# Performance work log

Measured on AMD Instinct MI355X. Metric: run time of the kernel, lower is better.

## Reference

```python
import jax, jax.numpy as jnp
import numpy as np

N = 200000      # active voxels
K = 27          # kernel volume (3x3x3)
M = 50000       # rulebook pairs per kernel offset
CIN = 64
COUT = 64


def setup_inputs() -> dict:
    key = jax.random.key(0)
    k1, k2, k3, k4 = jax.random.split(key, 4)
    feats = jax.random.normal(k1, (N, CIN), dtype=jnp.float32)
    std = 1.0 / np.sqrt(CIN * K)
    kernel = jax.random.uniform(k2, (K, CIN, COUT), dtype=jnp.float32,
                                minval=-std, maxval=std)
    in_map = jax.random.randint(k3, (K, M), 0, N, dtype=jnp.int32)
    out_map = jax.random.randint(k4, (K, M), 0, N, dtype=jnp.int32)
    return {"feats": feats, "kernel": kernel, "in_map": in_map, "out_map": out_map}


def reference(feats, kernel, in_map, out_map):
    # gather: [K, M, Cin]
    gathered = feats[in_map]
    # per-offset GEMM: [K, M, Cout]
    partial = jnp.einsum('kmi,kio->kmo', gathered, kernel)
    # scatter-add into output features [N, Cout]
    out = jnp.zeros((feats.shape[0], kernel.shape[-1]), dtype=feats.dtype)
    out = out.at[out_map].add(partial)
    return out
```

## Files before the change

kernel.cpp:

```cpp
#include <hip/hip_runtime.h>

#define CIN  64
#define COUT 64

typedef __attribute__((ext_vector_type(8))) short bf16x8;
typedef __attribute__((ext_vector_type(4))) float f32x4;

__global__ __launch_bounds__(256)
void zero_out_kernel(float4* __restrict__ out, int n4) {
    int i = blockIdx.x * 256 + threadIdx.x;
    if (i < n4) out[i] = make_float4(0.f, 0.f, 0.f, 0.f);
}

__device__ inline unsigned short f2bf(float f) {
    unsigned u = __float_as_uint(f);
    return (unsigned short)((u + 0x7FFFu + ((u >> 16) & 1u)) >> 16);
}

__global__ __launch_bounds__(256)
void spconv_mfma(const float* __restrict__ feats,
                 const float* __restrict__ weight,
                 const int*   __restrict__ in_map,
                 const int*   __restrict__ out_map,
                 float*       __restrict__ out,
                 int M) {
    const int k     = blockIdx.y;
    const int tid   = threadIdx.x;
    const int lane  = tid & 63;
    const int m     = lane & 15;
    const int quad  = lane >> 4;
    const int wave  = blockIdx.x * 4 + (tid >> 6);
    const int nwaves = gridDim.x * 4;

    const float* __restrict__ wk = weight + (size_t)k * (CIN * COUT);
    bf16x8 bfrag[4][2];
#pragma unroll
    for (int t = 0; t < 4; ++t) {
#pragma unroll
        for (int h = 0; h < 2; ++h) {
            const int n = 16 * t + m;
            const int c0 = 32 * h + 8 * quad;
#pragma unroll
            for (int j = 0; j < 8; ++j)
                bfrag[t][h][j] = (short)f2bf(wk[(c0 + j) * COUT + n]);
        }
    }

    const int base   = k * M;
    const int ntiles = M >> 4;

    for (int tile = wave; tile < ntiles; tile += nwaves) {
        const int p0 = tile << 4;

        const int in_row  = in_map[base + p0 + m];
        const int out_row = out_map[base + p0 + m];

        const float* __restrict__ fr = feats + (size_t)in_row * CIN + 8 * quad;
        const f32x4 f0 = *(const f32x4*)(fr + 0);
        const f32x4 f1 = *(const f32x4*)(fr + 4);
        const f32x4 f2 = *(const f32x4*)(fr + 32);
        const f32x4 f3 = *(const f32x4*)(fr + 36);

        bf16x8 a0, a1;
#pragma unroll
        for (int j = 0; j < 4; ++j) {
            a0[j]     = (short)f2bf(f0[j]);
            a0[j + 4] = (short)f2bf(f1[j]);
            a1[j]     = (short)f2bf(f2[j]);
            a1[j + 4] = (short)f2bf(f3[j]);
        }

        int orow[4];
#pragma unroll
        for (int r = 0; r < 4; ++r)
            orow[r] = __shfl(out_row, 4 * quad + r);

        f32x4 acc[4];
#pragma unroll
        for (int t = 0; t < 4; ++t) {
            acc[t] = {0.f, 0.f, 0.f, 0.f};
            acc[t] = __builtin_amdgcn_mfma_f32_16x16x32_bf16(a0, bfrag[t][0], acc[t], 0, 0, 0);
            acc[t] = __builtin_amdgcn_mfma_f32_16x16x32_bf16(a1, bfrag[t][1], acc[t], 0, 0, 0);
        }

#pragma unroll
        for (int t = 0; t < 4; ++t)
#pragma unroll
            for (int r = 0; r < 4; ++r)
                atomicAdd(out + (size_t)orow[r] * COUT + 16 * t + m, acc[t][r]);
    }
}

extern "C" void kernel_launch(void* const* d_in, const int* in_sizes, int n_in,
                              void* d_out, int out_size, void* d_ws, size_t ws_size,
                              hipStream_t stream) {
    const float* feats   = (const float*)d_in[0];
    const float* weight  = (const float*)d_in[1];
    const int*   in_map  = (const int*)d_in[2];
    const int*   out_map = (const int*)d_in[3];
    float*       out     = (float*)d_out;

    const int K = in_sizes[1] / (CIN * COUT);
    const int M = in_sizes[2] / K;

    {
        int n4 = out_size / 4;
        zero_out_kernel<<<(n4 + 255) / 256, 256, 0, stream>>>((float4*)out, n4);
    }

    dim3 grid(64, K);
    spconv_mfma<<<grid, 256, 0, stream>>>(feats, weight, in_map, out_map, out, M);
}
```

Measured before the change: 377.6 us.

## Pair lanes via shuffles to issue packed two-float atomic adds

Adjacent lanes swap accumulator values with xor-shuffles so each lane holds two consecutive output columns for one row. Each lane then issues a packed v2f32 global atomic add, halving the number of atomic operations per tile. The change also replaces the custom zeroing kernel with hipMemsetAsync and raises the grid from 64 to 80 blocks per kernel offset. In exchange it adds shuffle and select overhead, and on toolchains without the builtin it falls back to two scalar atomics.

```diff
diff --git a/kernel.cpp b/kernel.cpp
--- a/kernel.cpp
+++ b/kernel.cpp
@@ -5,16 +5,22 @@
 
 typedef __attribute__((ext_vector_type(8))) short bf16x8;
 typedef __attribute__((ext_vector_type(4))) float f32x4;
-
-__global__ __launch_bounds__(256)
-void zero_out_kernel(float4* __restrict__ out, int n4) {
-    int i = blockIdx.x * 256 + threadIdx.x;
-    if (i < n4) out[i] = make_float4(0.f, 0.f, 0.f, 0.f);
-}
+typedef __attribute__((ext_vector_type(2))) float f32x2;
 
 __device__ inline unsigned short f2bf(float f) {
     unsigned u = __float_as_uint(f);
     return (unsigned short)((u + 0x7FFFu + ((u >> 16) & 1u)) >> 16);
+}
+
+__device__ inline void atomic_pk_add(float* addr, f32x2 v) {
+#if __has_builtin(__builtin_amdgcn_global_atomic_fadd_v2f32)
+    typedef __attribute__((address_space(1))) f32x2 gf32x2;
+    __builtin_amdgcn_global_atomic_fadd_v2f32(
+        (gf32x2*)(unsigned long long)(void*)addr, v);
+#else
+    atomicAdd(addr + 0, v.x);
+    atomicAdd(addr + 1, v.y);
+#endif
 }
 
 __global__ __launch_bounds__(256)
@@ -83,11 +89,26 @@
             acc[t] = __builtin_amdgcn_mfma_f32_16x16x32_bf16(a1, bfrag[t][1], acc[t], 0, 0, 0);
         }
 
+        const bool odd = (m & 1);
 #pragma unroll
-        for (int t = 0; t < 4; ++t)
-#pragma unroll
-            for (int r = 0; r < 4; ++r)
-                atomicAdd(out + (size_t)orow[r] * COUT + 16 * t + m, acc[t][r]);
+        for (int t = 0; t < 4; ++t) {
+            const float pv0 = __shfl_xor(acc[t][0], 1);
+            const float pv1 = __shfl_xor(acc[t][1], 1);
+            const float pv2 = __shfl_xor(acc[t][2], 1);
+            const float pv3 = __shfl_xor(acc[t][3], 1);
+            const int colb = 16 * t + (m & ~1);
+
+            const int ra = odd ? orow[2] : orow[0];
+            const int rb = odd ? orow[3] : orow[1];
+            f32x2 va, vb;
+            va.x = odd ? pv2       : acc[t][0];
+            va.y = odd ? acc[t][2] : pv0;
+            vb.x = odd ? pv3       : acc[t][1];
+            vb.y = odd ? acc[t][3] : pv1;
+
+            atomic_pk_add(out + (size_t)ra * COUT + colb, va);
+            atomic_pk_add(out + (size_t)rb * COUT + colb, vb);
+        }
     }
 }
 
@@ -103,11 +124,8 @@
     const int K = in_sizes[1] / (CIN * COUT);
     const int M = in_sizes[2] / K;
 
-    {
-        int n4 = out_size / 4;
-        zero_out_kernel<<<(n4 + 255) / 256, 256, 0, stream>>>((float4*)out, n4);
-    }
+    hipMemsetAsync(out, 0, (size_t)out_size * sizeof(float), stream);
 
-    dim3 grid(64, K);
+    dim3 grid(80, K);
     spconv_mfma<<<grid, 256, 0, stream>>>(feats, weight, in_map, out_map, out, M);
 }
```

Result: slower. 651.4 us (+72.5%).

## Replace atomic scatter-add with inverse-index gather using fp16 partials

Applied to the files above, without the earlier changes.

Builds an inverse rulebook (a per-output-row count plus a capped pair list) with a cheap atomic pass. Phase 1 computes the per-pair GEMM with MFMA and stores the results as fp16 partials in the workspace. Phase 2 has one wave per output row sum its partials and write the row once, which removes the zeroing pass and the per-element float atomics. In exchange the code writes and reads a large partial buffer, loses precision by storing partials in fp16, and silently drops any contributions past CAP=48 per output row. It falls back to the atomic path when the workspace is too small.

```diff
diff --git a/kernel.cpp b/kernel.cpp
--- a/kernel.cpp
+++ b/kernel.cpp
@@ -1,16 +1,12 @@
 #include <hip/hip_runtime.h>
+#include <hip/hip_fp16.h>
 
 #define CIN  64
 #define COUT 64
+#define CAP  48
 
 typedef __attribute__((ext_vector_type(8))) short bf16x8;
 typedef __attribute__((ext_vector_type(4))) float f32x4;
-
-__global__ __launch_bounds__(256)
-void zero_out_kernel(float4* __restrict__ out, int n4) {
-    int i = blockIdx.x * 256 + threadIdx.x;
-    if (i < n4) out[i] = make_float4(0.f, 0.f, 0.f, 0.f);
-}
 
 __device__ inline unsigned short f2bf(float f) {
     unsigned u = __float_as_uint(f);
@@ -18,42 +14,48 @@
 }
 
 __global__ __launch_bounds__(256)
-void spconv_mfma(const float* __restrict__ feats,
-                 const float* __restrict__ weight,
-                 const int*   __restrict__ in_map,
-                 const int*   __restrict__ out_map,
-                 float*       __restrict__ out,
-                 int M) {
-    const int k     = blockIdx.y;
-    const int tid   = threadIdx.x;
-    const int lane  = tid & 63;
-    const int m     = lane & 15;
-    const int quad  = lane >> 4;
-    const int wave  = blockIdx.x * 4 + (tid >> 6);
+void build_inverse(const int* __restrict__ out_map, int total,
+                   int* __restrict__ cnt, int* __restrict__ pairlist) {
+    int g = blockIdx.x * 256 + threadIdx.x;
+    if (g >= total) return;
+    int r = out_map[g];
+    int pos = atomicAdd(&cnt[r], 1);
+    if (pos < CAP) pairlist[r * CAP + pos] = g;
+}
+
+__global__ __launch_bounds__(256)
+void spconv_phase1(const float* __restrict__ feats,
+                   const float* __restrict__ weight,
+                   const int*   __restrict__ in_map,
+                   __half*      __restrict__ partial,
+                   int M) {
+    const int k      = blockIdx.y;
+    const int tid    = threadIdx.x;
+    const int lane   = tid & 63;
+    const int m      = lane & 15;
+    const int quad   = lane >> 4;
+    const int wave   = blockIdx.x * 4 + (tid >> 6);
     const int nwaves = gridDim.x * 4;
 
     const float* __restrict__ wk = weight + (size_t)k * (CIN * COUT);
     bf16x8 bfrag[4][2];
 #pragma unroll
-    for (int t = 0; t < 4; ++t) {
+    for (int t = 0; t < 4; ++t)
 #pragma unroll
         for (int h = 0; h < 2; ++h) {
-            const int n = 16 * t + m;
+            const int n  = 16 * t + m;
             const int c0 = 32 * h + 8 * quad;
 #pragma unroll
             for (int j = 0; j < 8; ++j)
                 bfrag[t][h][j] = (short)f2bf(wk[(c0 + j) * COUT + n]);
         }
-    }
 
     const int base   = k * M;
     const int ntiles = M >> 4;
 
     for (int tile = wave; tile < ntiles; tile += nwaves) {
         const int p0 = tile << 4;
-
-        const int in_row  = in_map[base + p0 + m];
-        const int out_row = out_map[base + p0 + m];
+        const int in_row = in_map[base + p0 + m];
 
         const float* __restrict__ fr = feats + (size_t)in_row * CIN + 8 * quad;
         const f32x4 f0 = *(const f32x4*)(fr + 0);
@@ -70,11 +72,6 @@
             a1[j + 4] = (short)f2bf(f3[j]);
         }
 
-        int orow[4];
-#pragma unroll
-        for (int r = 0; r < 4; ++r)
-            orow[r] = __shfl(out_row, 4 * quad + r);
-
         f32x4 acc[4];
 #pragma unroll
         for (int t = 0; t < 4; ++t) {
@@ -83,12 +80,118 @@
             acc[t] = __builtin_amdgcn_mfma_f32_16x16x32_bf16(a1, bfrag[t][1], acc[t], 0, 0, 0);
         }
 
+        const size_t tbase = ((size_t)(k * ntiles + tile) << 10) + 256 * quad + m;
+#pragma unroll
+        for (int t = 0; t < 4; ++t)
+#pragma unroll
+            for (int r = 0; r < 4; ++r)
+                partial[tbase + 64 * r + 16 * t] = __float2half(acc[t][r]);
+    }
+}
+
+__global__ __launch_bounds__(256)
+void spconv_phase2(const __half* __restrict__ partial,
+                   const int*    __restrict__ cnt,
+                   const int*    __restrict__ pairlist,
+                   float*        __restrict__ out,
+                   int nrows) {
+    const int lane   = threadIdx.x & 63;
+    const int wave   = blockIdx.x * 4 + (threadIdx.x >> 6);
+    const int nwaves = gridDim.x * 4;
+
+    for (int r = wave; r < nrows; r += nwaves) {
+        int c = cnt[r];
+        if (c > CAP) c = CAP;
+        const int* __restrict__ pl = pairlist + r * CAP;
+
+        float acc = 0.f;
+        for (int j = 0; j < c; ++j) {
+            const int e   = pl[j];
+            const int r15 = e & 15;
+            const size_t elem = ((size_t)(e >> 4) << 10)
+                              + 256 * (r15 >> 2) + 64 * (r15 & 3) + lane;
+            acc += __half2float(partial[elem]);
+        }
+        out[(size_t)r * COUT + lane] = acc;
+    }
+}
+
+__global__ __launch_bounds__(256)
+void spconv_atomic(const float* __restrict__ feats,
+                   const float* __restrict__ weight,
+                   const int*   __restrict__ in_map,
+                   const int*   __restrict__ out_map,
+                   float*       __restrict__ out,
+                   int M) {
+    const int k      = blockIdx.y;
+    const int tid    = threadIdx.x;
+    const int lane   = tid & 63;
+    const int m      = lane & 15;
+    const int quad   = lane >> 4;
+    const int wave   = blockIdx.x * 4 + (tid >> 6);
+    const int nwaves = gridDim.x * 4;
+
+    const float* __restrict__ wk = weight + (size_t)k * (CIN * COUT);
+    bf16x8 bfrag[4][2];
+#pragma unroll
+    for (int t = 0; t < 4; ++t)
+#pragma unroll
+        for (int h = 0; h < 2; ++h) {
+            const int n  = 16 * t + m;
+            const int c0 = 32 * h + 8 * quad;
+#pragma unroll
+            for (int j = 0; j < 8; ++j)
+                bfrag[t][h][j] = (short)f2bf(wk[(c0 + j) * COUT + n]);
+        }
+
+    const int base   = k * M;
+    const int ntiles = M >> 4;
+
+    for (int tile = wave; tile < ntiles; tile += nwaves) {
+        const int p0 = tile << 4;
+        const int in_row  = in_map[base + p0 + m];
+        const int out_row = out_map[base + p0 + m];
+
+        const float* __restrict__ fr = feats + (size_t)in_row * CIN + 8 * quad;
+        const f32x4 f0 = *(const f32x4*)(fr + 0);
+        const f32x4 f1 = *(const f32x4*)(fr + 4);
+        const f32x4 f2 = *(const f32x4*)(fr + 32);
+        const f32x4 f3 = *(const f32x4*)(fr + 36);
+
+        bf16x8 a0, a1;
+#pragma unroll
+        for (int j = 0; j < 4; ++j) {
+            a0[j]     = (short)f2bf(f0[j]);
+            a0[j + 4] = (short)f2bf(f1[j]);
+            a1[j]     = (short)f2bf(f2[j]);
+            a1[j + 4] = (short)f2bf(f3[j]);
+        }
+
+        int orow[4];
+#pragma unroll
+        for (int r = 0; r < 4; ++r)
+            orow[r] = __shfl(out_row, 4 * quad + r);
+
+        f32x4 acc[4];
+#pragma unroll
+        for (int t = 0; t < 4; ++t) {
+            acc[t] = {0.f, 0.f, 0.f, 0.f};
+            acc[t] = __builtin_amdgcn_mfma_f32_16x16x32_bf16(a0, bfrag[t][0], acc[t], 0, 0, 0);
+            acc[t] = __builtin_amdgcn_mfma_f32_16x16x32_bf16(a1, bfrag[t][1], acc[t], 0, 0, 0);
+        }
+
 #pragma unroll
         for (int t = 0; t < 4; ++t)
 #pragma unroll
             for (int r = 0; r < 4; ++r)
                 atomicAdd(out + (size_t)orow[r] * COUT + 16 * t + m, acc[t][r]);
     }
+}
+
+__global__ __launch_bounds__(256)
+void zero_out_kernel(float4* __restrict__ out, int n4) {
+    int i = blockIdx.x * 256 + threadIdx.x;
+    if (i < n4) out[i] = make_float4(0.f, 0.f, 0.f, 0.f);
 }
 
 extern "C" void kernel_launch(void* const* d_in, const int* in_sizes, int n_in,
@@ -100,14 +203,35 @@
     const int*   out_map = (const int*)d_in[3];
     float*       out     = (float*)d_out;
 
-    const int K = in_sizes[1] / (CIN * COUT);
-    const int M = in_sizes[2] / K;
-
-    {
+    const int K     = in_sizes[1] / (CIN * COUT);
+    const int M     = in_sizes[2] / K;
+    const int N     = out_size / COUT;
+    const int total = K * M;
+
+    const size_t cnt_b  = ((size_t)N * 4 + 255) & ~(size_t)255;
+    const size_t pl_b   = ((size_t)N * CAP * 4 + 255) & ~(size_t)255;
+    const size_t part_b = (size_t)total * COUT * sizeof(__half);
+    const size_t need   = cnt_b + pl_b + part_b;
+
+    if ((M & 15) == 0 && ws_size >= need) {
+        int*    cnt      = (int*)d_ws;
+        int*    pairlist = (int*)((char*)d_ws + cnt_b);
+        __half* partial  = (__half*)((char*)d_ws + cnt_b + pl_b);
+
+        hipMemsetAsync(cnt, 0, (size_t)N * 4, stream);
+
+        build_inverse<<<(total + 255) / 256, 256, 0, stream>>>(
+            out_map, total, cnt, pairlist);
+
+        dim3 g1(80, K);
+        spconv_phase1<<<g1, 256, 0, stream>>>(feats, weight, in_map, partial, M);
+
+        spconv_phase2<<<2048, 256, 0, stream>>>(partial, cnt, pairlist, out, N);
+    } else {
         int n4 = out_size / 4;
         zero_out_kernel<<<(n4 + 255) / 256, 256, 0, stream>>>((float4*)out, n4);
-    }
-
-    dim3 grid(64, K);
-    spconv_mfma<<<grid, 256, 0, stream>>>(feats, weight, in_map, out_map, out, M);
-}
+        dim3 grid(80, K);
+        spconv_atomic<<<grid, 256, 0, stream>>>(
+            feats, weight, in_map, out_map, out, M);
+    }
+}
```

Result: slower. 510.2 us (+35.1%).

## Accumulate scatter-add in packed fp16 atomics with pre-converted bf16 features

Applied to the files above, without the earlier changes.

Adds a path that first converts all features to bf16 in workspace, then runs the MFMA gather-GEMM and scatters results with packed v2f16 global atomics into an fp16 accumulator, which is converted back to fp32 at the end. Lanes exchange values via shuffles so each atomic carries two adjacent output columns, halving the number of atomics and the bytes moved in gathers and scatters. The grid also grows from 64 to 80 blocks per offset. It adds extra conversion passes and a memset, and fp16 accumulation risks precision loss and overflow relative to the fp32 reference.

```diff
diff --git a/kernel.cpp b/kernel.cpp
--- a/kernel.cpp
+++ b/kernel.cpp
@@ -1,16 +1,18 @@
 #include <hip/hip_runtime.h>
-
-#define CIN  64
-#define COUT 64
-
-typedef __attribute__((ext_vector_type(8))) short bf16x8;
-typedef __attribute__((ext_vector_type(4))) float f32x4;
-
-__global__ __launch_bounds__(256)
-void zero_out_kernel(float4* __restrict__ out, int n4) {
-    int i = blockIdx.x * 256 + threadIdx.x;
-    if (i < n4) out[i] = make_float4(0.f, 0.f, 0.f, 0.f);
-}
+#include <hip/hip_fp16.h>
+
+#define CIN   64
+#define COUT  64
+
+typedef __attribute__((ext_vector_type(8))) short    bf16x8;
+typedef __attribute__((ext_vector_type(4))) float    f32x4;
+typedef __attribute__((ext_vector_type(2))) _Float16 f16x2;
+
+#if __has_builtin(__builtin_amdgcn_global_atomic_fadd_v2f16)
+#define HAVE_PK16 1
+#else
+#define HAVE_PK16 0
+#endif
 
 __device__ inline unsigned short f2bf(float f) {
     unsigned u = __float_as_uint(f);
@@ -18,44 +20,147 @@
 }
 
 __global__ __launch_bounds__(256)
-void spconv_mfma(const float* __restrict__ feats,
-                 const float* __restrict__ weight,
-                 const int*   __restrict__ in_map,
-                 const int*   __restrict__ out_map,
-                 float*       __restrict__ out,
-                 int M) {
-    const int k     = blockIdx.y;
-    const int tid   = threadIdx.x;
-    const int lane  = tid & 63;
-    const int m     = lane & 15;
-    const int quad  = lane >> 4;
-    const int wave  = blockIdx.x * 4 + (tid >> 6);
+void cvt_feats(const float4* __restrict__ in, unsigned short* __restrict__ outb,
+               int n8) {
+    int i = blockIdx.x * 256 + threadIdx.x;
+    if (i >= n8) return;
+    float4 f0 = in[2 * i], f1 = in[2 * i + 1];
+    bf16x8 o;
+    o[0] = (short)f2bf(f0.x); o[1] = (short)f2bf(f0.y);
+    o[2] = (short)f2bf(f0.z); o[3] = (short)f2bf(f0.w);
+    o[4] = (short)f2bf(f1.x); o[5] = (short)f2bf(f1.y);
+    o[6] = (short)f2bf(f1.z); o[7] = (short)f2bf(f1.w);
+    *(bf16x8*)(outb + 8 * (size_t)i) = o;
+}
+
+__global__ __launch_bounds__(256)
+void cvt_out(const __half2* __restrict__ hacc, float2* __restrict__ out, int n2) {
+    int i = blockIdx.x * 256 + threadIdx.x;
+    if (i >= n2) return;
+    const __half2 h = hacc[i];
+    out[i] = make_float2(__half2float(__low2half(h)), __half2float(__high2half(h)));
+}
+
+#if HAVE_PK16
+__global__ __launch_bounds__(256)
+void spconv_pk(const unsigned short* __restrict__ featsb,
+               const float*          __restrict__ weight,
+               const int*            __restrict__ in_map,
+               const int*            __restrict__ out_map,
+               __half*               __restrict__ hacc,
+               int M) {
+    const int k      = blockIdx.y;
+    const int tid    = threadIdx.x;
+    const int lane   = tid & 63;
+    const int m      = lane & 15;
+    const int quad   = lane >> 4;
+    const int wave   = blockIdx.x * 4 + (tid >> 6);
     const int nwaves = gridDim.x * 4;
+    const bool odd   = (m & 1);
 
     const float* __restrict__ wk = weight + (size_t)k * (CIN * COUT);
     bf16x8 bfrag[4][2];
 #pragma unroll
-    for (int t = 0; t < 4; ++t) {
+    for (int t = 0; t < 4; ++t)
 #pragma unroll
         for (int h = 0; h < 2; ++h) {
-            const int n = 16 * t + m;
+            const int n  = 16 * t + m;
             const int c0 = 32 * h + 8 * quad;
 #pragma unroll
             for (int j = 0; j < 8; ++j)
                 bfrag[t][h][j] = (short)f2bf(wk[(c0 + j) * COUT + n]);
         }
-    }
 
     const int base   = k * M;
     const int ntiles = M >> 4;
 
+    typedef __attribute__((address_space(1))) f16x2 gf16x2;
+    f16x2* const hacc2 = (f16x2*)hacc;
+
+    for (int tile = wave; tile < ntiles; tile += nwaves) {
+        const int p0      = tile << 4;
+        const int in_row  = in_map[base + p0 + m];
+        const int out_row = out_map[base + p0 + m];
+
+        const unsigned short* fb = featsb + ((size_t)in_row << 6) + 8 * quad;
+        const bf16x8 a0 = *(const bf16x8*)fb;
+        const bf16x8 a1 = *(const bf16x8*)(fb + 32);
+
+        int orow[4];
+#pragma unroll
+        for (int r = 0; r < 4; ++r)
+            orow[r] = __shfl(out_row, 4 * quad + r);
+
+        f32x4 acc[4];
+#pragma unroll
+        for (int t = 0; t < 4; ++t) {
+            acc[t] = {0.f, 0.f, 0.f, 0.f};
+            acc[t] = __builtin_amdgcn_mfma_f32_16x16x32_bf16(a0, bfrag[t][0], acc[t], 0, 0, 0);
+            acc[t] = __builtin_amdgcn_mfma_f32_16x16x32_bf16(a1, bfrag[t][1], acc[t], 0, 0, 0);
+        }
+
+        const int coldw = m >> 1;
+        const int ra = odd ? orow[2] : orow[0];
+        const int rb = odd ? orow[3] : orow[1];
+#pragma unroll
+        for (int t = 0; t < 4; ++t) {
+            const float send0 = odd ? acc[t][0] : acc[t][2];
+            const float send1 = odd ? acc[t][1] : acc[t][3];
+            const float recv0 = __shfl_xor(send0, 1);
+            const float recv1 = __shfl_xor(send1, 1);
+
+            f16x2 va, vb;
+            va[0] = (_Float16)(odd ? recv0 : acc[t][0]);
+            va[1] = (_Float16)(odd ? acc[t][2] : recv0);
+            vb[0] = (_Float16)(odd ? recv1 : acc[t][1]);
+            vb[1] = (_Float16)(odd ? acc[t][3] : recv1);
+
+            __builtin_amdgcn_global_atomic_fadd_v2f16(
+                (gf16x2*)(unsigned long long)(void*)&hacc2[(size_t)ra * 32 + coldw + 8 * t], va);
+            __builtin_amdgcn_global_atomic_fadd_v2f16(
+                (gf16x2*)(unsigned long long)(void*)&hacc2[(size_t)rb * 32 + coldw + 8 * t], vb);
+        }
+    }
+}
+#endif
+
+__global__ __launch_bounds__(256)
+void spconv_atomic(const float* __restrict__ feats,
+                   const float* __restrict__ weight,
+                   const int*   __restrict__ in_map,
+                   const int*   __restrict__ out_map,
+                   float*       __restrict__ out,
+                   int M) {
+    const int k      = blockIdx.y;
+    const int tid    = threadIdx.x;
+    const int lane   = tid & 63;
+    const int m      = lane & 15;
+    const int quad   = lane >> 4;
+    const int wave   = blockIdx.x * 4 + (tid >> 6);
+    const int nwaves = gridDim.x * 4;
+
+    const float* __restrict__ wk = weight + (size_t)k * (CIN * COUT);
+    bf16x8 bfrag[4][2];
+#pragma unroll
+    for (int t = 0; t < 4; ++t)
+#pragma unroll
+        for (int h = 0; h < 2; ++h) {
+            const int n  = 16 * t + m;
+            const int c0 = 32 * h + 8 * quad;
+#pragma unroll
+            for (int j = 0; j < 8; ++j)
+                bfrag[t][h][j] = (short)f2bf(wk[(c0 + j) * COUT + n]);
+        }
+
+    const int base   = k * M;
+    const int ntiles = M >> 4;
+
     for (int tile = wave; tile < ntiles; tile += nwaves) {
         const int p0 = tile << 4;
-
         const int in_row  = in_map[base + p0 + m];
         const int out_row = out_map[base + p0 + m];
 
-        const float* __restrict__ fr = feats + (size_t)in_row * CIN + 8 * quad;
+        const float* __restrict__ fr = feats + ((size_t)in_row << 6) + 8 * quad;
         const f32x4 f0 = *(const f32x4*)(fr + 0);
         const f32x4 f1 = *(const f32x4*)(fr + 4);
         const f32x4 f2 = *(const f32x4*)(fr + 32);
@@ -89,6 +194,12 @@
             for (int r = 0; r < 4; ++r)
                 atomicAdd(out + (size_t)orow[r] * COUT + 16 * t + m, acc[t][r]);
     }
+}
+
+__global__ __launch_bounds__(256)
+void zero_out_kernel(float4* __restrict__ out, int n4) {
+    int i = blockIdx.x * 256 + threadIdx.x;
+    if (i < n4) out[i] = make_float4(0.f, 0.f, 0.f, 0.f);
 }
 
 extern "C" void kernel_launch(void* const* d_in, const int* in_sizes, int n_in,
@@ -102,12 +213,35 @@
 
     const int K = in_sizes[1] / (CIN * COUT);
     const int M = in_sizes[2] / K;
-
-    {
-        int n4 = out_size / 4;
-        zero_out_kernel<<<(n4 + 255) / 256, 256, 0, stream>>>((float4*)out, n4);
+    const int N = out_size / COUT;
+
+    const size_t fb_b   = ((size_t)N * CIN * 2 + 255) & ~(size_t)255;
+    const size_t hacc_b = (size_t)N * COUT * 2;
+    const size_t need   = fb_b + hacc_b;
+
+#if HAVE_PK16
+    if ((M & 15) == 0 && ws_size >= need) {
+        unsigned short* featsb = (unsigned short*)d_ws;
+        __half*         hacc   = (__half*)((char*)d_ws + fb_b);
+
+        hipMemsetAsync(hacc, 0, hacc_b, stream);
+
+        const int n8 = N * CIN / 8;
+        cvt_feats<<<(n8 + 255) / 256, 256, 0, stream>>>(
+            (const float4*)feats, featsb, n8);
+
+        dim3 grid(80, K);
+        spconv_pk<<<grid, 256, 0, stream>>>(featsb, weight, in_map, out_map,
+                                            hacc, M);
+
+        const int n2 = N * COUT / 2;
+        cvt_out<<<(n2 + 255) / 256, 256, 0, stream>>>(
+            (const __half2*)hacc, (float2*)out, n2);
+        return;
     }
-
-    dim3 grid(64, K);
-    spconv_mfma<<<grid, 256, 0, stream>>>(feats, weight, in_map, out_map, out, M);
-}
+#endif
+    int n4 = out_size / 4;
+    zero_out_kernel<<<(n4 + 255) / 256, 256, 0, stream>>>((float4*)out, n4);
+    dim3 grid(80, K);
+    spconv_atomic<<<grid, 256, 0, stream>>>(feats, weight, in_map, out_map, out, M);
+}
```

New measurement: 374.4 us. About the same (-0.9%).
